# Optimization experiments

Hardware: AMD Instinct MI355X
Metric: run time of the kernel (lower is better)

Reference implementation:

```python
import jax, jax.numpy as jnp
import numpy as np

D_MODEL = 1024
N_HEADS = 16
DH = D_MODEL // N_HEADS            # 64
Q_PROJ = D_MODEL // 2              # 512
KV_PROJ = 2 * D_MODEL // 3         # 682
LN_EPS = 1e-5                      # torch.nn.LayerNorm default


def _layernorm(x, gamma, beta, eps=LN_EPS):
    mu = jnp.mean(x, axis=-1, keepdims=True)
    var = jnp.mean(jnp.square(x - mu), axis=-1, keepdims=True)
    return (x - mu) * jax.lax.rsqrt(var + eps) * gamma + beta


def setup_inputs() -> dict:
    key = jax.random.key(0)
    ks = jax.random.split(key, 6)
    B, L = 2, 2048
    x = jax.random.normal(ks[0], (B, L, D_MODEL), dtype=jnp.float32)
    W_dq = 0.01 * jax.random.normal(ks[1], (D_MODEL, Q_PROJ), dtype=jnp.float32)
    W_uq = 0.01 * jax.random.normal(ks[2], (Q_PROJ, D_MODEL), dtype=jnp.float32)
    W_dkv = 0.01 * jax.random.normal(ks[3], (D_MODEL, KV_PROJ), dtype=jnp.float32)
    W_ukv = 0.01 * jax.random.normal(ks[4], (KV_PROJ, 2 * D_MODEL), dtype=jnp.float32)
    q_gamma = jnp.ones((Q_PROJ,), jnp.float32)
    q_beta = jnp.zeros((Q_PROJ,), jnp.float32)
    kv_gamma = jnp.ones((KV_PROJ,), jnp.float32)
    kv_beta = jnp.zeros((KV_PROJ,), jnp.float32)
    return {"x": x, "W_dq": W_dq, "W_uq": W_uq, "q_gamma": q_gamma,
            "q_beta": q_beta, "W_dkv": W_dkv, "W_ukv": W_ukv,
            "kv_gamma": kv_gamma, "kv_beta": kv_beta}


def reference(x, W_dq, W_uq, q_gamma, q_beta, W_dkv, W_ukv, kv_gamma, kv_beta):
    B, L, _ = x.shape
    # low-rank Q path: down-project, layernorm, up-project
    compressed_q = _layernorm(x @ W_dq, q_gamma, q_beta)      # [B,L,Q_PROJ]
    Q = compressed_q @ W_uq                                    # [B,L,D]
    # low-rank joint KV path
    compressed_kv = _layernorm(x @ W_dkv, kv_gamma, kv_beta)  # [B,L,KV_PROJ]
    KV = compressed_kv @ W_ukv                                 # [B,L,2D]
    K, V = KV[..., :D_MODEL], KV[..., D_MODEL:]
    # split heads: [B,H,L,dh]
    q = Q.reshape(B, L, N_HEADS, DH).transpose(0, 2, 1, 3)
    k = K.reshape(B, L, N_HEADS, DH).transpose(0, 2, 1, 3)
    v = V.reshape(B, L, N_HEADS, DH).transpose(0, 2, 1, 3)
    scores = jnp.einsum('bhqd,bhkd->bhqk', q, k) / jnp.sqrt(jnp.float32(DH))
    attn = jax.nn.softmax(scores, axis=-1)                     # [B,H,L,L]
    # NOTE: original forward computes feat = LN(dropout(fc(attn@v)) + x) but
    # discards it, returning (x, attn, compressed_kv). Dead code omitted.
    return (x, attn, compressed_kv)
```

## Files before the change

### kernel.cpp

```cpp
#include <hip/hip_runtime.h>

typedef __bf16 bf16;
typedef __bf16 bf16x4 __attribute__((ext_vector_type(4)));
typedef __bf16 bf16x8 __attribute__((ext_vector_type(8)));
typedef float f32x4 __attribute__((ext_vector_type(4)));

#define GCAST(p) ((const __attribute__((address_space(1))) void*)(p))
#define LCAST(p) ((__attribute__((address_space(3))) void*)(p))

#define ML 4096
#define DM 1024
#define QP 512
#define KVP 682
#define KVPP 768
#define NDOWN 1280

__device__ __forceinline__ void trans_tile(const float* __restrict__ src, int srcLD,
                                           int K, int N, int NP,
                                           bf16* __restrict__ dst, int dstLD, int dn,
                                           int bx, int by, float (*tile)[65]) {
    const int k0 = bx * 64, n0 = by * 64;
    const int c = threadIdx.x & 63, r4 = threadIdx.x >> 6;
    #pragma unroll
    for (int rr = r4; rr < 64; rr += 4) {
        int k = k0 + rr, n = n0 + c;
        tile[rr][c] = (k < K && n < N) ? src[(size_t)k * srcLD + n] : 0.f;
    }
    __syncthreads();
    #pragma unroll
    for (int nn = r4; nn < 64; nn += 4) {
        int n = n0 + nn, k = k0 + c;
        if (n < NP && k < dstLD)
            dst[(size_t)(n + dn) * dstLD + k] = (bf16)tile[c][nn];
    }
}

__global__ __launch_bounds__(256) void prep(const f32x4* __restrict__ x4,
                                            f32x4* __restrict__ out0,
                                            bf16* __restrict__ xb,
                                            const float* __restrict__ Wdq,
                                            const float* __restrict__ Wdkv,
                                            const float* __restrict__ Wuq,
                                            const float* __restrict__ Wukv,
                                            bf16* __restrict__ Wdt,
                                            bf16* __restrict__ Wuqt,
                                            bf16* __restrict__ Wukvt) {
    __shared__ float tile[64][65];
    int bid = blockIdx.x;
    if (bid < 4096) {
        int i = bid * 256 + threadIdx.x;
        f32x4 v = x4[i];
        __builtin_nontemporal_store(v, &out0[i]);
        bf16x4 b;
        b[0] = (bf16)v.x; b[1] = (bf16)v.y; b[2] = (bf16)v.z; b[3] = (bf16)v.w;
        *(bf16x4*)(xb + (size_t)i * 4) = b;
        return;
    }
    int rel = bid - 4096;
    if (rel < 128) {
        trans_tile(Wdq, QP, DM, QP, QP, Wdt, DM, 0, rel & 15, rel >> 4, tile);
    } else if (rel < 320) {
        rel -= 128;
        trans_tile(Wdkv, KVP, DM, KVP, KVPP, Wdt, DM, QP, rel & 15, rel >> 4, tile);
    } else if (rel < 448) {
        rel -= 320;
        trans_tile(Wuq, DM, QP, DM, DM, Wuqt, QP, 0, rel & 7, rel >> 3, tile);
    } else {
        rel -= 448;
        trans_tile(Wukv, 2048, KVP, DM, DM, Wukvt, KVPP, 0, rel % 12, rel / 12, tile);
    }
}

__device__ __forceinline__ void gemm_body(const bf16* __restrict__ A,
                                          const bf16* __restrict__ Bt,
                                          bf16* __restrict__ C,
                                          int N, int K, int bx, int by,
                                          bf16* As, bf16* Bs) {
    const int t = threadIdx.x;
    const int w = t >> 6, lane = t & 63;
    const int bm = bx * 128, bn = by * 128;
    const int wr = (w >> 1) * 64, wc = (w & 1) * 64;
    const int r16 = lane & 15, g4 = lane >> 4;
    const int srow = w * 16 + (lane >> 2);
    const int scol = (lane & 3) * 8;

    f32x4 acc[4][4] = {};

    for (int k0 = 0; k0 < K; k0 += 32) {
        #pragma unroll
        for (int r = 0; r < 2; ++r) {
            const bf16* ga = A + (size_t)(bm + r*64 + srow) * K + k0 + scol;
            __builtin_amdgcn_global_load_lds(GCAST(ga), LCAST(&As[r*2048 + w*512]), 16, 0, 0);
            const bf16* gb = Bt + (size_t)(bn + r*64 + srow) * K + k0 + scol;
            __builtin_amdgcn_global_load_lds(GCAST(gb), LCAST(&Bs[r*2048 + w*512]), 16, 0, 0);
        }
        __syncthreads();
        bf16x8 af[4], bfr[4];
        #pragma unroll
        for (int i = 0; i < 4; ++i)
            af[i] = *(const bf16x8*)&As[(wr + i*16 + r16) * 32 + g4*8];
        #pragma unroll
        for (int j = 0; j < 4; ++j)
            bfr[j] = *(const bf16x8*)&Bs[(wc + j*16 + r16) * 32 + g4*8];
        #pragma unroll
        for (int i = 0; i < 4; ++i)
            #pragma unroll
            for (int j = 0; j < 4; ++j)
                acc[i][j] = __builtin_amdgcn_mfma_f32_16x16x32_bf16(af[i], bfr[j], acc[i][j], 0, 0, 0);
        __syncthreads();
    }
    #pragma unroll
    for (int i = 0; i < 4; ++i)
        #pragma unroll
        for (int j = 0; j < 4; ++j)
            #pragma unroll
            for (int r = 0; r < 4; ++r) {
                int row = bm + wr + i*16 + g4*4 + r;
                int col = bn + wc + j*16 + r16;
                C[(size_t)row * N + col] = (bf16)acc[i][j][r];
            }
}

__global__ __launch_bounds__(256) void gemm_down(const bf16* __restrict__ A,
                                                 const bf16* __restrict__ Bt,
                                                 bf16* __restrict__ C) {
    __shared__ bf16 As[128 * 32];
    __shared__ bf16 Bs[128 * 32];
    gemm_body(A, Bt, C, NDOWN, DM, blockIdx.x, blockIdx.y, As, Bs);
}

__global__ __launch_bounds__(256) void gemm_up2(const bf16* __restrict__ Cq,
                                                const bf16* __restrict__ Wuqt,
                                                bf16* __restrict__ Qb,
                                                const bf16* __restrict__ Ckv,
                                                const bf16* __restrict__ Wukvt,
                                                bf16* __restrict__ Kb) {
    __shared__ bf16 As[128 * 32];
    __shared__ bf16 Bs[128 * 32];
    if (blockIdx.z == 0)
        gemm_body(Cq,  Wuqt,  Qb, DM, QP,   blockIdx.x, blockIdx.y, As, Bs);
    else
        gemm_body(Ckv, Wukvt, Kb, DM, KVPP, blockIdx.x, blockIdx.y, As, Bs);
}

__device__ __forceinline__ void block_reduce2(float& s, float& sq) {
    #pragma unroll
    for (int m = 1; m < 64; m <<= 1) {
        s  += __shfl_xor(s, m);
        sq += __shfl_xor(sq, m);
    }
    __shared__ float ls[4], lq[4];
    int w = threadIdx.x >> 6;
    __syncthreads();
    if ((threadIdx.x & 63) == 0) { ls[w] = s; lq[w] = sq; }
    __syncthreads();
    s  = ls[0] + ls[1] + ls[2] + ls[3];
    sq = lq[0] + lq[1] + lq[2] + lq[3];
}

__global__ __launch_bounds__(256) void ln_fused(const bf16* __restrict__ Cdown,
                                                const float* __restrict__ qg,
                                                const float* __restrict__ qb,
                                                const float* __restrict__ kvg,
                                                const float* __restrict__ kvb,
                                                bf16* __restrict__ Cq,
                                                float* __restrict__ out2,
                                                bf16* __restrict__ Ckv) {
    const int row = blockIdx.x, t = threadIdx.x;
    const bf16* src = Cdown + (size_t)row * NDOWN;

    {
        float v0 = (float)src[t], v1 = (float)src[t + 256];
        float s = v0 + v1, sq = v0*v0 + v1*v1;
        block_reduce2(s, sq);
        float mu = s * (1.f/512.f);
        float var = sq * (1.f/512.f) - mu*mu;
        float rs = rsqrtf(var + 1e-5f);
        Cq[(size_t)row*QP + t]       = (bf16)((v0 - mu)*rs*qg[t]     + qb[t]);
        Cq[(size_t)row*QP + t + 256] = (bf16)((v1 - mu)*rs*qg[t+256] + qb[t+256]);
    }
    {
        const bf16* skv = src + QP;
        float v[3];
        float s = 0.f, sq = 0.f;
        #pragma unroll
        for (int i = 0; i < 3; ++i) {
            int j = t + i*256;
            v[i] = (j < KVP) ? (float)skv[j] : 0.f;
            s += v[i]; sq += v[i]*v[i];
        }
        block_reduce2(s, sq);
        float mu = s * (1.f/682.f);
        float var = sq * (1.f/682.f) - mu*mu;
        float rs = rsqrtf(var + 1e-5f);
        #pragma unroll
        for (int i = 0; i < 3; ++i) {
            int j = t + i*256;
            if (j < KVP) {
                float y = (v[i]-mu)*rs*kvg[j] + kvb[j];
                __builtin_nontemporal_store(y, &out2[(size_t)row*KVP + j]);
                Ckv[(size_t)row*KVPP + j] = (bf16)y;
            } else if (j < KVPP) {
                Ckv[(size_t)row*KVPP + j] = (bf16)0.f;
            }
        }
    }
}

__global__ __launch_bounds__(512, 2) void attn_k(const bf16* __restrict__ Qb,
                                                 const bf16* __restrict__ Kb,
                                                 float* __restrict__ out1) {
    __shared__ bf16 Qs[16 * 64];
    __shared__ float reds[8][16];
    __shared__ bf16 P[16 * 2048];

    const int t = threadIdx.x, w = t >> 6, lane = t & 63;
    const int flat = blockIdx.x;
    const int xcd = flat & 7, local = flat >> 3;
    const int qblk = local & 127;
    const int bh = (xcd << 2) | (local >> 7);
    const int b = bh >> 4, h = bh & 15;
    const int q0 = qblk * 16;

    for (int i = t; i < 1024; i += 512) {
        int qr = i >> 6, d = i & 63;
        Qs[i] = Qb[(size_t)(b*2048 + q0 + qr) * DM + h*64 + d];
    }
    __syncthreads();

    const int r16 = lane & 15, g4 = lane >> 4;
    bf16x8 qf0 = *(const bf16x8*)&Qs[r16*64 + g4*8];
    bf16x8 qf1 = *(const bf16x8*)&Qs[r16*64 + 32 + g4*8];

    const bf16* kbase = Kb + (size_t)b * 2048 * DM + h*64;
    const int colw = w * 256;

    float sm = 0.f;
    #pragma unroll
    for (int ni = 0; ni < 16; ++ni) {
        const bf16* kr = kbase + (size_t)(colw + ni*16 + r16) * DM + g4*8;
        bf16x8 k0 = *(const bf16x8*)kr;
        bf16x8 k1 = *(const bf16x8*)(kr + 32);
        f32x4 c = {};
        c = __builtin_amdgcn_mfma_f32_16x16x32_bf16(k0, qf0, c, 0, 0, 0);
        c = __builtin_amdgcn_mfma_f32_16x16x32_bf16(k1, qf1, c, 0, 0, 0);
        bf16x4 pv;
        #pragma unroll
        for (int r = 0; r < 4; ++r) {
            float e = __expf(c[r] * 0.125f);
            sm += e;
            pv[r] = (bf16)e;
        }
        int byte = (r16*4096 + colw*2 + ni*32 + g4*8) ^ ((r16 & 7) << 4);
        *(bf16x4*)((char*)P + byte) = pv;
    }
    sm += __shfl_xor(sm, 16);
    sm += __shfl_xor(sm, 32);
    if (g4 == 0) reds[w][r16] = sm;
    __syncthreads();

    #pragma unroll
    for (int rr = 0; rr < 2; ++rr) {
        int row = w * 2 + rr;
        float s = 0.f;
        #pragma unroll
        for (int ww = 0; ww < 8; ++ww) s += reds[ww][row];
        float inv = 1.f / s;
        float* rowout = out1 + ((size_t)(bh * 2048 + q0 + row)) * 2048;
        const char* rowp = (const char*)P + row * 4096;
        const int xr = (row & 7) << 4;
        #pragma unroll
        for (int c = 0; c < 8; ++c) {
            int byte = (c*512 + lane*8) ^ xr;
            bf16x4 pv = *(const bf16x4*)(rowp + byte);
            f32x4 v;
            v[0] = (float)pv[0] * inv;
            v[1] = (float)pv[1] * inv;
            v[2] = (float)pv[2] * inv;
            v[3] = (float)pv[3] * inv;
            __builtin_nontemporal_store(v, (f32x4*)(rowout + c*256 + lane*4));
        }
    }
}

extern "C" void kernel_launch(void* const* d_in, const int* in_sizes, int n_in,
                              void* d_out, int out_size, void* d_ws, size_t ws_size,
                              hipStream_t stream) {
    const float* x    = (const float*)d_in[0];
    const float* Wdq  = (const float*)d_in[1];
    const float* Wuq  = (const float*)d_in[2];
    const float* qg   = (const float*)d_in[3];
    const float* qbt  = (const float*)d_in[4];
    const float* Wdkv = (const float*)d_in[5];
    const float* Wukv = (const float*)d_in[6];
    const float* kvg  = (const float*)d_in[7];
    const float* kvb  = (const float*)d_in[8];

    float* out0 = (float*)d_out;
    float* out1 = out0 + (size_t)4194304;
    float* out2 = out1 + (size_t)134217728;

    char* ws = (char*)d_ws;
    bf16* Xbf   = (bf16*)(ws + 0);
    bf16* Wdt   = (bf16*)(ws + 8388608);
    bf16* Wuqt  = (bf16*)(ws + 11010048);
    bf16* Wukvt = (bf16*)(ws + 12058624);
    bf16* Cdown = (bf16*)(ws + 13631488);
    bf16* Cq    = (bf16*)(ws + 24117248);
    bf16* Ckv   = (bf16*)(ws + 28311552);
    bf16* Qb    = (bf16*)(ws + 34603008);
    bf16* Kb    = (bf16*)(ws + 42991616);

    prep<<<4736, 256, 0, stream>>>((const f32x4*)x, (f32x4*)out0, Xbf,
                                   Wdq, Wdkv, Wuq, Wukv, Wdt, Wuqt, Wukvt);
    gemm_down<<<dim3(ML/128, NDOWN/128), 256, 0, stream>>>(Xbf, Wdt, Cdown);
    ln_fused<<<ML, 256, 0, stream>>>(Cdown, qg, qbt, kvg, kvb, Cq, out2, Ckv);
    gemm_up2<<<dim3(ML/128, DM/128, 2), 256, 0, stream>>>(Cq, Wuqt, Qb, Ckv, Wukvt, Kb);
    attn_k<<<4096, 512, 0, stream>>>(Qb, Kb, out1);
}
```

Measured before the change: 213.3 us.

## Double-buffer LDS tiles in projection GEMMs to overlap loads with MFMA

The shared GEMM body now ping-pongs between two LDS buffers: it issues the global-to-LDS loads for the next K-slice before running the MFMAs on the current slice, and needs one barrier per iteration instead of two. It also hoists the row pointer arithmetic out of the loop. The aim is to hide global load latency behind compute in the down and up projections. LDS use per block doubles, which may lower occupancy. Correctness depends on the single barrier being enough to order the async LDS writes against the reads of the other buffer.

```diff
diff --git a/kernel.cpp b/kernel.cpp
--- a/kernel.cpp
+++ b/kernel.cpp
@@ -84,31 +84,52 @@
     const int srow = w * 16 + (lane >> 2);
     const int scol = (lane & 3) * 8;
 
+    const bf16* gA = A + (size_t)(bm + srow) * K + scol;
+    const bf16* gB = Bt + (size_t)(bn + srow) * K + scol;
+    const size_t rstep = (size_t)64 * K;
+
     f32x4 acc[4][4] = {};
 
-    for (int k0 = 0; k0 < K; k0 += 32) {
-        #pragma unroll
-        for (int r = 0; r < 2; ++r) {
-            const bf16* ga = A + (size_t)(bm + r*64 + srow) * K + k0 + scol;
-            __builtin_amdgcn_global_load_lds(GCAST(ga), LCAST(&As[r*2048 + w*512]), 16, 0, 0);
-            const bf16* gb = Bt + (size_t)(bn + r*64 + srow) * K + k0 + scol;
-            __builtin_amdgcn_global_load_lds(GCAST(gb), LCAST(&Bs[r*2048 + w*512]), 16, 0, 0);
-        }
+    #define STAGE(buf, k0)                                                        \
+        {                                                                         \
+            _Pragma("unroll")                                                     \
+            for (int r = 0; r < 2; ++r) {                                         \
+                __builtin_amdgcn_global_load_lds(GCAST(gA + r*rstep + (k0)),      \
+                    LCAST(&As[(buf)*4096 + r*2048 + w*512]), 16, 0, 0);           \
+                __builtin_amdgcn_global_load_lds(GCAST(gB + r*rstep + (k0)),      \
+                    LCAST(&Bs[(buf)*4096 + r*2048 + w*512]), 16, 0, 0);           \
+            }                                                                     \
+        }
+
+    #define COMPUTE(buf)                                                          \
+        {                                                                         \
+            bf16x8 af[4], bfr[4];                                                 \
+            _Pragma("unroll")                                                     \
+            for (int i = 0; i < 4; ++i)                                           \
+                af[i] = *(const bf16x8*)&As[(buf)*4096 + (wr + i*16 + r16) * 32 + g4*8]; \
+            _Pragma("unroll")                                                     \
+            for (int j = 0; j < 4; ++j)                                           \
+                bfr[j] = *(const bf16x8*)&Bs[(buf)*4096 + (wc + j*16 + r16) * 32 + g4*8]; \
+            _Pragma("unroll")                                                     \
+            for (int i = 0; i < 4; ++i)                                           \
+                _Pragma("unroll")                                                 \
+                for (int j = 0; j < 4; ++j)                                       \
+                    acc[i][j] = __builtin_amdgcn_mfma_f32_16x16x32_bf16(af[i], bfr[j], acc[i][j], 0, 0, 0); \
+        }
+
+    STAGE(0, 0);
+    __syncthreads();
+    int cur = 0;
+    for (int k0 = 32; k0 < K; k0 += 32) {
+        STAGE(cur ^ 1, k0);
+        COMPUTE(cur);
         __syncthreads();
-        bf16x8 af[4], bfr[4];
-        #pragma unroll
-        for (int i = 0; i < 4; ++i)
-            af[i] = *(const bf16x8*)&As[(wr + i*16 + r16) * 32 + g4*8];
-        #pragma unroll
-        for (int j = 0; j < 4; ++j)
-            bfr[j] = *(const bf16x8*)&Bs[(wc + j*16 + r16) * 32 + g4*8];
-        #pragma unroll
-        for (int i = 0; i < 4; ++i)
-            #pragma unroll
-            for (int j = 0; j < 4; ++j)
-                acc[i][j] = __builtin_amdgcn_mfma_f32_16x16x32_bf16(af[i], bfr[j], acc[i][j], 0, 0, 0);
-        __syncthreads();
-    }
+        cur ^= 1;
+    }
+    COMPUTE(cur);
+    #undef STAGE
+    #undef COMPUTE
+
     #pragma unroll
     for (int i = 0; i < 4; ++i)
         #pragma unroll
@@ -124,8 +145,8 @@
 __global__ __launch_bounds__(256) void gemm_down(const bf16* __restrict__ A,
                                                  const bf16* __restrict__ Bt,
                                                  bf16* __restrict__ C) {
-    __shared__ bf16 As[128 * 32];
-    __shared__ bf16 Bs[128 * 32];
+    __shared__ bf16 As[2 * 128 * 32];
+    __shared__ bf16 Bs[2 * 128 * 32];
     gemm_body(A, Bt, C, NDOWN, DM, blockIdx.x, blockIdx.y, As, Bs);
 }
 
@@ -135,8 +156,8 @@
                                                 const bf16* __restrict__ Ckv,
                                                 const bf16* __restrict__ Wukvt,
                                                 bf16* __restrict__ Kb) {
-    __shared__ bf16 As[128 * 32];
-    __shared__ bf16 Bs[128 * 32];
+    __shared__ bf16 As[2 * 128 * 32];
+    __shared__ bf16 Bs[2 * 128 * 32];
     if (blockIdx.z == 0)
         gemm_body(Cq,  Wuqt,  Qb, DM, QP,   blockIdx.x, blockIdx.y, As, Bs);
     else
```

Measured after the change: 221.3 us. 3.8% more time.

## Fuse Q up-projection into attention kernel, drop Q GEMM pass

Applied to the files above, without the earlier changes.

Q is no longer produced by the up-projection GEMM and written to workspace. Instead, each attention block computes its own 16x64 Q tile directly from compressed Q and the Q up-projection weights using MFMA, done by four waves before the score loop. This removes half of the up-projection launch and the Q round trip through global memory. In exchange, each attention block does a K=512 mini-GEMM with unshared global loads, while the other four waves sit idle at the barrier.

```diff
diff --git a/kernel.cpp b/kernel.cpp
--- a/kernel.cpp
+++ b/kernel.cpp
@@ -129,18 +129,12 @@
     gemm_body(A, Bt, C, NDOWN, DM, blockIdx.x, blockIdx.y, As, Bs);
 }
 
-__global__ __launch_bounds__(256) void gemm_up2(const bf16* __restrict__ Cq,
-                                                const bf16* __restrict__ Wuqt,
-                                                bf16* __restrict__ Qb,
-                                                const bf16* __restrict__ Ckv,
+__global__ __launch_bounds__(256) void gemm_upK(const bf16* __restrict__ Ckv,
                                                 const bf16* __restrict__ Wukvt,
                                                 bf16* __restrict__ Kb) {
     __shared__ bf16 As[128 * 32];
     __shared__ bf16 Bs[128 * 32];
-    if (blockIdx.z == 0)
-        gemm_body(Cq,  Wuqt,  Qb, DM, QP,   blockIdx.x, blockIdx.y, As, Bs);
-    else
-        gemm_body(Ckv, Wukvt, Kb, DM, KVPP, blockIdx.x, blockIdx.y, As, Bs);
+    gemm_body(Ckv, Wukvt, Kb, DM, KVPP, blockIdx.x, blockIdx.y, As, Bs);
 }
 
 __device__ __forceinline__ void block_reduce2(float& s, float& sq) {
@@ -207,7 +201,8 @@
     }
 }
 
-__global__ __launch_bounds__(512, 2) void attn_k(const bf16* __restrict__ Qb,
+__global__ __launch_bounds__(512, 2) void attn_k(const bf16* __restrict__ Cq,
+                                                 const bf16* __restrict__ Wuqt,
                                                  const bf16* __restrict__ Kb,
                                                  float* __restrict__ out1) {
     __shared__ bf16 Qs[16 * 64];
@@ -221,14 +216,24 @@
     const int bh = (xcd << 2) | (local >> 7);
     const int b = bh >> 4, h = bh & 15;
     const int q0 = qblk * 16;
-
-    for (int i = t; i < 1024; i += 512) {
-        int qr = i >> 6, d = i & 63;
-        Qs[i] = Qb[(size_t)(b*2048 + q0 + qr) * DM + h*64 + d];
-    }
-    __syncthreads();
-
     const int r16 = lane & 15, g4 = lane >> 4;
+
+    if (w < 4) {
+        const bf16* arow = Cq + (size_t)(b*2048 + q0 + r16) * QP + g4*8;
+        const bf16* brow = Wuqt + (size_t)(h*64 + w*16 + r16) * QP + g4*8;
+        f32x4 qa = {};
+        #pragma unroll
+        for (int ks = 0; ks < 16; ++ks) {
+            bf16x8 aa = *(const bf16x8*)(arow + ks*32);
+            bf16x8 bb = *(const bf16x8*)(brow + ks*32);
+            qa = __builtin_amdgcn_mfma_f32_16x16x32_bf16(aa, bb, qa, 0, 0, 0);
+        }
+        #pragma unroll
+        for (int r = 0; r < 4; ++r)
+            Qs[(g4*4 + r) * 64 + w*16 + r16] = (bf16)qa[r];
+    }
+    __syncthreads();
+
     bf16x8 qf0 = *(const bf16x8*)&Qs[r16*64 + g4*8];
     bf16x8 qf1 = *(const bf16x8*)&Qs[r16*64 + 32 + g4*8];
 
@@ -308,13 +313,12 @@
     bf16* Cdown = (bf16*)(ws + 13631488);
     bf16* Cq    = (bf16*)(ws + 24117248);
     bf16* Ckv   = (bf16*)(ws + 28311552);
-    bf16* Qb    = (bf16*)(ws + 34603008);
     bf16* Kb    = (bf16*)(ws + 42991616);
 
     prep<<<4736, 256, 0, stream>>>((const f32x4*)x, (f32x4*)out0, Xbf,
                                    Wdq, Wdkv, Wuq, Wukv, Wdt, Wuqt, Wukvt);
     gemm_down<<<dim3(ML/128, NDOWN/128), 256, 0, stream>>>(Xbf, Wdt, Cdown);
     ln_fused<<<ML, 256, 0, stream>>>(Cdown, qg, qbt, kvg, kvb, Cq, out2, Ckv);
-    gemm_up2<<<dim3(ML/128, DM/128, 2), 256, 0, stream>>>(Cq, Wuqt, Qb, Ckv, Wukvt, Kb);
-    attn_k<<<4096, 512, 0, stream>>>(Qb, Kb, out1);
-}
+    gemm_upK<<<dim3(ML/128, DM/128), 256, 0, stream>>>(Ckv, Wukvt, Kb);
+    attn_k<<<4096, 512, 0, stream>>>(Cq, Wuqt, Kb, out1);
+}
```

Result: slower. 266.7 us (+25.0%).
